# Optimization experiments

Hardware: AMD Instinct MI355X
Metric: run time of the kernel (lower is better)

The kernel has to match this reference:

```python
import jax, jax.numpy as jnp
import numpy as np

HEADS = 16
SEQ_LEN = 1024
MEM_LEN = 1024
CMEM_LEN = 256
CMEM_RATIO = 4


def _shift(x):
    # x: [b, h, i, j] -> relative position shift trick, output [b, h, i, j]
    b, h, i, j = x.shape
    x = jnp.concatenate([x, jnp.zeros((b, h, i, i), x.dtype)], -1)
    l = i + j - 1
    flat = x.reshape(b, h, -1)
    pad = (-flat.shape[-1]) % l
    flat = jnp.concatenate([flat, jnp.zeros((b, h, pad), x.dtype)], -1)
    return flat.reshape(b, h, -1, l)[..., :i, i - 1:]


def _full_attn(q, k, v):
    scale = q.shape[-1] ** -0.5
    a = jax.nn.softmax(jnp.einsum('bhid,bhjd->bhij', q, k) * scale, -1)
    return jnp.einsum('bhij,bhjd->bhid', a, v)


def setup_inputs() -> dict:
    key = jax.random.key(0)
    ks = jax.random.split(key, 10)
    b, t, e = 4, SEQ_LEN, 1024
    d = e // HEADS
    kv_len = CMEM_LEN + MEM_LEN + t
    s = 0.02
    return {
        'x': jax.random.normal(ks[0], (b, t, e), jnp.float32),
        'mem': jax.random.normal(ks[1], (b, MEM_LEN, e), jnp.float32),
        'cmem': jax.random.normal(ks[2], (b, CMEM_LEN, e), jnp.float32),
        'pos_emb': jax.random.normal(ks[3], (HEADS, kv_len, d), jnp.float32),
        'input_mask': jnp.ones((b, t), bool),
        'Wq': jax.random.normal(ks[4], (e, e), jnp.float32) * s,
        'Wkv': jax.random.normal(ks[5], (e, 2 * e), jnp.float32) * s,
        'Wout': jax.random.normal(ks[6], (e, e), jnp.float32) * s,
        'bout': jnp.zeros((e,), jnp.float32),
        'conv_w': jax.random.normal(ks[7], (e, e, CMEM_RATIO), jnp.float32) * s,
        'conv_b': jnp.zeros((e,), jnp.float32),
    }


def reference(x, mem, cmem, pos_emb, input_mask, Wq, Wkv, Wout, bout, conv_w, conv_b):
    b, t, e = x.shape
    h = HEADS
    d = e // h
    scale = d ** -0.5
    ml, cml = mem.shape[1], cmem.shape[1]

    q = x @ Wq                                      # [b, t, e]
    kv_input = jnp.concatenate([cmem, mem, x], 1)   # [b, kv_len, e]
    k, v = jnp.split(kv_input @ Wkv, 2, -1)

    mh = lambda u: u.reshape(b, -1, h, d).transpose(0, 2, 1, 3)
    q, k, v = mh(q), mh(k), mh(v)                   # [b, h, n, d]
    kv_len = k.shape[2]

    dots = jnp.einsum('bhid,bhjd->bhij', q, k) * scale
    neg = -jnp.finfo(dots.dtype).max

    pe = pos_emb[:, -kv_len:].astype(q.dtype)
    pos_dots = _shift(jnp.einsum('bhid,hjd->bhij', q, pe) * scale)
    dots = dots + pos_dots

    # padding mask (True where attention allowed), pad mem+cmem region with True
    pad_mask = input_mask[:, None, :, None] & input_mask[:, None, None, :]
    pad_mask = jnp.pad(pad_mask, ((0, 0), (0, 0), (0, 0), (ml + cml, 0)), constant_values=True)
    dots = jnp.where(pad_mask, dots, neg)

    total_mem = ml + cml
    causal = jnp.triu(jnp.ones((t, t + total_mem), bool), k=1 + total_mem)
    dots = jnp.where(causal[None, None], neg, dots)

    attn = jax.nn.softmax(dots, -1)
    out = jnp.einsum('bhij,bhjd->bhid', attn, v).transpose(0, 2, 1, 3).reshape(b, t, e)
    logits = out @ Wout + bout

    # --- memory update (t == seq_len, calc_memory=True) ---
    mem_cat = jnp.concatenate([mem, x], 1)          # [b, ml+t, e]
    old_mem, new_mem = mem_cat[:, :-MEM_LEN], mem_cat[:, -MEM_LEN:]
    # old_mem length (t) is divisible by CMEM_RATIO, no pad needed
    xm = old_mem.reshape(b, -1, CMEM_RATIO, e)
    compressed = jnp.einsum('bmri,oir->bmo', xm, conv_w) + conv_b  # Conv1d k=stride=ratio
    cmem_cat = jnp.concatenate([cmem, compressed], 1)
    new_cmem = cmem_cat[:, -CMEM_LEN:]

    # --- auxiliary reconstruction loss (all operands detached) ---
    ck, cv = jnp.split(compressed @ Wkv, 2, -1)
    ck, cv = mh(ck), mh(cv)
    start = kv_len - min(ml, MEM_LEN) - SEQ_LEN
    end = kv_len - SEQ_LEN
    omk, omv = k[:, :, start:end], v[:, :, start:end]
    sg = jax.lax.stop_gradient
    q2, omk, omv, ck, cv = map(sg, (q, omk, omv, ck, cv))
    aux_loss = jnp.mean((_full_attn(q2, omk, omv) - _full_attn(q2, ck, cv)) ** 2)

    return logits, new_mem, new_cmem, aux_loss
```

## Files before the change

### kernel.cpp

```cpp
#include <hip/hip_runtime.h>
#include <hip/hip_bf16.h>
#include <cstddef>

typedef unsigned short u16;
typedef __attribute__((ext_vector_type(8))) short bf16x8;
typedef __attribute__((ext_vector_type(4))) float f32x4;

#define C2 0.18033688011112042f

__device__ __forceinline__ u16 f2b(float f) {
    unsigned u = __builtin_bit_cast(unsigned, f);
    unsigned r = (u + 0x7FFF + ((u >> 16) & 1)) >> 16;
    return (u16)r;
}

__device__ __forceinline__ float exp2a(float x) {
    float r; asm("v_exp_f32 %0, %1" : "=v"(r) : "v"(x)); return r;
}

__device__ __forceinline__ unsigned cvtpk(float lo, float hi) {
    unsigned r; asm("v_cvt_pk_bf16_f32 %0, %1, %2" : "=v"(r) : "v"(lo), "v"(hi));
    return r;
}

__device__ __forceinline__ void gload_lds16(const void* g, void* l) {
    __builtin_amdgcn_global_load_lds(
        (const __attribute__((address_space(1))) unsigned int*)g,
        (__attribute__((address_space(3))) unsigned int*)l, 16, 0, 0);
}

#define VDRAIN() asm volatile("s_waitcnt vmcnt(0)" ::: "memory")
#define SBAR() do { __builtin_amdgcn_sched_barrier(0); __builtin_amdgcn_s_barrier(); } while (0)

__device__ __forceinline__ void transpose_body(
    const float* __restrict__ in, u16* __restrict__ out, int K, int N,
    int bx, int by, float (*t)[33], int tid)
{
    int k0 = by * 32, n0 = bx * 32;
    int tx = tid & 31, ty = tid >> 5;
    #pragma unroll
    for (int p = 0; p < 4; ++p)
        t[ty + 8 * p][tx] = in[(size_t)(k0 + ty + 8 * p) * N + n0 + tx];
    __syncthreads();
    #pragma unroll
    for (int p = 0; p < 4; ++p)
        out[(size_t)(n0 + ty + 8 * p) * K + k0 + tx] = f2b(t[tx][ty + 8 * p]);
}

__global__ __launch_bounds__(256) void megaprep(
    const float* __restrict__ pos, u16* __restrict__ peb,
    const float* __restrict__ x, const float* __restrict__ mem,
    const float* __restrict__ cmem, u16* __restrict__ kvin,
    const float* __restrict__ Wkv, u16* __restrict__ wkvt,
    const float* __restrict__ Wq, u16* __restrict__ wqt,
    const float* __restrict__ Wout, u16* __restrict__ woutt,
    const float* __restrict__ convw, u16* __restrict__ w2t)
{
    __shared__ float t[32][33];
    const int bid = blockIdx.x, tid = threadIdx.x;
    if (bid < 2304) {
        int i = bid * 256 + tid;
        float4 v = ((const float4*)pos)[i];
        union { u16 s[4]; uint2 u; } pk;
        pk.s[0] = f2b(v.x); pk.s[1] = f2b(v.y); pk.s[2] = f2b(v.z); pk.s[3] = f2b(v.w);
        ((uint2*)peb)[i] = pk.u;
    } else if (bid < 11520) {
        int rowg = bid - 2304;
        int b = rowg / 2304, rr = rowg % 2304;
        const float* src = (rr < 256)  ? cmem + ((size_t)b * 256 + rr) * 1024
                         : (rr < 1280) ? mem  + ((size_t)b * 1024 + (rr - 256)) * 1024
                                       : x    + ((size_t)b * 1024 + (rr - 1280)) * 1024;
        float4 v = ((const float4*)src)[tid];
        union { u16 s[4]; uint2 u; } pk;
        pk.s[0] = f2b(v.x); pk.s[1] = f2b(v.y); pk.s[2] = f2b(v.z); pk.s[3] = f2b(v.w);
        ((uint2*)(kvin + (size_t)rowg * 1024))[tid] = pk.u;
    } else if (bid < 13568) {
        int m = bid - 11520;
        transpose_body(Wkv, wkvt, 1024, 2048, m % 64, m / 64, t, tid);
    } else if (bid < 14592) {
        int m = bid - 13568;
        transpose_body(Wq, wqt, 1024, 1024, m % 32, m / 32, t, tid);
    } else if (bid < 15616) {
        int m = bid - 14592;
        transpose_body(Wout, woutt, 1024, 1024, m % 32, m / 32, t, tid);
    } else {
        int m = bid - 15616;
        int pidx = m * 256 + tid;
        int o = pidx >> 10, i = pidx & 1023;
        float4 v = *(const float4*)(convw + ((size_t)o << 12) + 4 * i);
        size_t base = (size_t)o * 4096 + i;
        w2t[base]          = f2b(v.x);
        w2t[base + 1024]   = f2b(v.y);
        w2t[base + 2048]   = f2b(v.z);
        w2t[base + 3072]   = f2b(v.w);
    }
}

__global__ __launch_bounds__(256) void transpose_v2(
    const u16* __restrict__ src1, u16* __restrict__ dst1,
    const u16* __restrict__ src2, u16* __restrict__ dst2)
{
    __shared__ u16 t[64 * 65];
    const int bid = blockIdx.x, tid = threadIdx.x;
    const u16* src; u16* dst; int R, bh, j0;
    if (bid < 2304) { src = src1; dst = dst1; R = 2304; bh = bid / 36; j0 = (bid % 36) * 64; }
    else { int m = bid - 2304; src = src2; dst = dst2; R = 256; bh = m / 4; j0 = (m % 4) * 64; }
    const int b = bh >> 4, h = bh & 15;
    #pragma unroll
    for (int p = 0; p < 2; ++p) {
        int idx = tid + p * 256;
        int j = idx >> 3, c = idx & 7;
        uint4 v = *(const uint4*)(src + ((size_t)(b * R + j0 + j)) * 2048 + 1024 + h * 64 + c * 8);
        const u16* vv = (const u16*)&v;
        #pragma unroll
        for (int u2 = 0; u2 < 8; ++u2) t[j * 65 + c * 8 + u2] = vv[u2];
    }
    __syncthreads();
    #pragma unroll
    for (int p = 0; p < 2; ++p) {
        int idx = tid + p * 256;
        int jc = idx & 7, d = idx >> 3;
        union { u16 s[8]; uint4 u; } pk;
        #pragma unroll
        for (int u2 = 0; u2 < 8; ++u2) pk.s[u2] = t[(jc * 8 + u2) * 65 + d];
        *(uint4*)(dst + ((size_t)(bh * 64 + d)) * (size_t)R + j0 + jc * 8) = pk.u;
    }
}

__device__ __forceinline__ void gemm_body(
    const u16* __restrict__ A, const u16* __restrict__ Bt,
    const float* __restrict__ bias, float* __restrict__ Cf,
    u16* __restrict__ Cb, int N, int K, float cscale,
    int apad, int ashift, int nxshift, int nyper, int id,
    u16* Al, u16* Bl)
{
    const int tid = threadIdx.x, w = tid >> 6, lane = tid & 63;
    const int lr = lane & 15, lg = lane >> 4;
    const int xcd = id & 7, s = id >> 3;
    const int bx = s & ((1 << nxshift) - 1);
    const int by = nyper * xcd + (s >> nxshift);
    const int bm0 = by * 128, bn0 = bx * 128;
    const int wr = (w >> 1) * 64, wc = (w & 1) * 64;

    f32x4 acc[4][4];
    const f32x4 z = {0.f, 0.f, 0.f, 0.f};
    #pragma unroll
    for (int mb = 0; mb < 4; ++mb)
        #pragma unroll
        for (int nb = 0; nb < 4; ++nb) acc[mb][nb] = z;

    for (int k0 = 0; k0 < K; k0 += 32) {
        __syncthreads();
        #pragma unroll
        for (int q = 0; q < 2; ++q) {
            int chunk = w * 2 + q;
            int row = bm0 + chunk * 16 + (lane >> 2);
            int arow = row + ((row >> ashift) * apad);
            int sg = (lane & 3) * 8;
            gload_lds16(A + (size_t)arow * K + k0 + sg, &Al[chunk * 512]);
            gload_lds16(Bt + (size_t)(bn0 + chunk * 16 + (lane >> 2)) * K + k0 + sg, &Bl[chunk * 512]);
        }
        __syncthreads();
        bf16x8 af[4], bf[4];
        #pragma unroll
        for (int mb = 0; mb < 4; ++mb)
            af[mb] = *(const bf16x8*)&Al[(wr + mb * 16 + lr) * 32 + lg * 8];
        #pragma unroll
        for (int nb = 0; nb < 4; ++nb)
            bf[nb] = *(const bf16x8*)&Bl[(wc + nb * 16 + lr) * 32 + lg * 8];
        #pragma unroll
        for (int mb = 0; mb < 4; ++mb)
            #pragma unroll
            for (int nb = 0; nb < 4; ++nb)
                acc[mb][nb] = __builtin_amdgcn_mfma_f32_16x16x32_bf16(
                    af[mb], bf[nb], acc[mb][nb], 0, 0, 0);
    }

    #pragma unroll
    for (int mb = 0; mb < 4; ++mb)
        #pragma unroll
        for (int nb = 0; nb < 4; ++nb)
            #pragma unroll
            for (int jr = 0; jr < 4; ++jr) {
                int row = bm0 + wr + mb * 16 + lg * 4 + jr;
                int col = bn0 + wc + nb * 16 + lr;
                float v = acc[mb][nb][jr] + (bias ? bias[col] : 0.f);
                if (Cf) Cf[(size_t)row * N + col] = v;
                if (Cb) Cb[(size_t)row * N + col] = f2b(v * cscale);
            }
}

__global__ __launch_bounds__(256) void gemm_bf16(
    const u16* __restrict__ A, const u16* __restrict__ Bt,
    const float* __restrict__ bias, float* __restrict__ Cf,
    u16* __restrict__ Cb, int N, int K, float cscale,
    int apad, int ashift, int nxshift, int nyper)
{
    __shared__ u16 Al[128 * 32];
    __shared__ u16 Bl[128 * 32];
    gemm_body(A, Bt, bias, Cf, Cb, N, K, cscale, apad, ashift, nxshift, nyper,
              blockIdx.x, Al, Bl);
}

__global__ __launch_bounds__(256) void gemm_dual(
    const u16* Aa, const u16* Bta, const float* biasa, float* Cfa, u16* Cba,
    int Na, int Ka, float csa, int apa, int asa, int nxa, int nya, int split,
    const u16* Ab, const u16* Btb, const float* biasb, float* Cfb, u16* Cbb,
    int Nb, int Kb, float csb, int apb, int asb, int nxb, int nyb)
{
    __shared__ u16 Al[128 * 32];
    __shared__ u16 Bl[128 * 32];
    if ((int)blockIdx.x < split)
        gemm_body(Aa, Bta, biasa, Cfa, Cba, Na, Ka, csa, apa, asa, nxa, nya,
                  blockIdx.x, Al, Bl);
    else
        gemm_body(Ab, Btb, biasb, Cfb, Cbb, Nb, Kb, csb, apb, asb, nxb, nyb,
                  blockIdx.x - split, Al, Bl);
}

__global__ __launch_bounds__(256) void attn_main_fused(
    const u16* __restrict__ qb,
    const u16* __restrict__ kvb,
    const u16* __restrict__ vt,
    const u16* __restrict__ peb,
    const u16* __restrict__ ckcv,
    const u16* __restrict__ cvt,
    u16* __restrict__ outb,
    float* __restrict__ acc)
{
    __shared__ u16 kbuf[64 * 64];
    __shared__ u16 vbuf[64 * 64];
    __shared__ u16 pering[128 * 64];
    __shared__ u16 pls[4][1024];
    __shared__ float red[4];

    const int tid = threadIdx.x;
    const int w = tid >> 6, lane = tid & 63;
    const int lr = lane & 15, lg = lane >> 4;
    const int rl = lane >> 3, cch = lane & 7;
    const int id = blockIdx.x;
    const int slot = id >> 3;
    const int bh = (id & 7) + ((slot >> 4) << 3);
    const int b = bh >> 4, h = bh & 15;
    const int i0 = (15 - (slot & 15)) * 64;
    const int iw = i0 + 16 * w;
    const int jb0 = 960 - i0;

    const int lrh = lr >> 3, lrm = lr & 7;
    int pwidx[4], pridx[2];
    #pragma unroll
    for (int nb = 0; nb < 4; ++nb)
        pwidx[nb] = (((nb * 2 + lrh) ^ (lg * 2)) * 8) + lrm;
    #pragma unroll
    for (int ks = 0; ks < 2; ++ks)
        pridx[ks] = lr * 64 + (((ks * 4 + lg) ^ ((lr >> 2) * 2)) * 8);

    bf16x8 qf[2];
    #pragma unroll
    for (int ks = 0; ks < 2; ++ks)
        qf[ks] = *(const bf16x8*)(qb + ((size_t)(b * 1024 + iw + lr)) * 1024
                                  + h * 64 + ks * 32 + lg * 8);

    const f32x4 z = {0.f, 0.f, 0.f, 0.f};
    f32x4 od[4], od2[4];
    float lloc[4], ll2[4];
    #pragma unroll
    for (int nb = 0; nb < 4; ++nb) { od[nb] = z; od2[nb] = z; }
    #pragma unroll
    for (int jr = 0; jr < 4; ++jr) { lloc[jr] = 0.f; ll2[jr] = 0.f; }

    #pragma unroll
    for (int q = 0; q < 2; ++q) {
        int row = 16 * w + 8 * q + rl;
        gload_lds16(kvb + ((size_t)(b * 2304 + row)) * 2048 + h * 64 + ((cch ^ rl) * 8),
                    &kbuf[(16 * w + 8 * q) * 64]);
        gload_lds16(vt + ((size_t)(bh * 64 + row)) * 2304 + ((cch ^ rl) * 8),
                    &vbuf[(16 * w + 8 * q) * 64]);
    }
    #pragma unroll
    for (int q = 0; q < 4; ++q) {
        int rr = 32 * w + 8 * q;
        int a = jb0 + rr + rl;
        int srow = a > 2303 ? 2303 : a;
        gload_lds16(peb + ((size_t)(h * 2304 + srow)) * 64 + ((cch ^ rl) * 8),
                    &pering[((jb0 + rr) & 127) * 64]);
    }
    VDRAIN();
    __syncthreads();

    const int nt = ((i0 + 1343) >> 6) + 1;
    for (int t = 0; t < nt; ++t) {
        const int j0 = t * 64;
        const int jb = jb0 + j0;
        const bool more = (t + 1 < nt);

        f32x4 qk[4], qp[5];
        #pragma unroll
        for (int nb = 0; nb < 4; ++nb) qk[nb] = z;
        #pragma unroll
        for (int f = 0; f < 5; ++f) qp[f] = z;
        __builtin_amdgcn_s_setprio(1);
        #pragma unroll
        for (int ks = 0; ks < 2; ++ks) {
            #pragma unroll
            for (int nb = 0; nb < 4; ++nb) {
                int row = nb * 16 + lr;
                bf16x8 kb = *(const bf16x8*)&kbuf[row * 64 + (((4 * ks + lg) ^ (row & 7)) * 8)];
                qk[nb] = __builtin_amdgcn_mfma_f32_16x16x32_bf16(qf[ks], kb, qk[nb], 0, 0, 0);
            }
            #pragma unroll
            for (int f = 0; f < 5; ++f) {
                int rel = 48 - 16 * w + f * 16 + lr;
                int slotp = (jb + rel) & 127;
                bf16x8 pb = *(const bf16x8*)&pering[slotp * 64 + (((4 * ks + lg) ^ (slotp & 7)) * 8)];
                qp[f] = __builtin_amdgcn_mfma_f32_16x16x32_bf16(qf[ks], pb, qp[f], 0, 0, 0);
            }
        }
        __builtin_amdgcn_s_setprio(0);

        VDRAIN();
        SBAR();

        if (more) {
            const int j0n = j0 + 64;
            #pragma unroll
            for (int q = 0; q < 2; ++q) {
                int row = 16 * w + 8 * q + rl;
                gload_lds16(kvb + ((size_t)(b * 2304 + j0n + row)) * 2048 + h * 64 + ((cch ^ rl) * 8),
                            &kbuf[(16 * w + 8 * q) * 64]);
            }
            const int A0 = jb + 128;
            #pragma unroll
            for (int q = 0; q < 2; ++q) {
                int rr = A0 + 16 * w + 8 * q;
                int a = rr + rl;
                int srow = a > 2303 ? 2303 : a;
                gload_lds16(peb + ((size_t)(h * 2304 + srow)) * 64 + ((cch ^ rl) * 8),
                            &pering[(rr & 127) * 64]);
            }
        }

        const bool nomask = (j0 + 63 <= iw + 1280);
        #pragma unroll
        for (int jr = 0; jr < 4; ++jr) {
            const int r = lg * 4 + jr;
            const int ia = iw + r;
            const int src = (lane & 48) | ((lr + 15 - r) & 15);
            float rot0 = __shfl(qp[0][jr], src);
            float rot1 = __shfl(qp[1][jr], src);
            float rot2 = __shfl(qp[2][jr], src);
            float rot3 = __shfl(qp[3][jr], src);
            float rot4 = __shfl(qp[4][jr], src);
            const bool hi = (lr > r);
            float s0 = qk[0][jr] + (hi ? rot1 : rot0);
            float s1 = qk[1][jr] + (hi ? rot2 : rot1);
            float s2 = qk[2][jr] + (hi ? rot3 : rot2);
            float s3 = qk[3][jr] + (hi ? rot4 : rot3);
            if (!nomask) {
                s0 = (j0 + lr      <= ia + 1280) ? s0 : -1e30f;
                s1 = (j0 + lr + 16 <= ia + 1280) ? s1 : -1e30f;
                s2 = (j0 + lr + 32 <= ia + 1280) ? s2 : -1e30f;
                s3 = (j0 + lr + 48 <= ia + 1280) ? s3 : -1e30f;
            }
            float p0 = exp2a(s0), p1 = exp2a(s1);
            float p2 = exp2a(s2), p3 = exp2a(s3);
            unsigned pkA = cvtpk(p0, p1), pkB = cvtpk(p2, p3);
            u16* pw = &pls[w][r * 64];
            pw[pwidx[0]] = (u16)pkA; pw[pwidx[1]] = (u16)(pkA >> 16);
            pw[pwidx[2]] = (u16)pkB; pw[pwidx[3]] = (u16)(pkB >> 16);
            lloc[jr] += (p0 + p1) + (p2 + p3);
        }

        __builtin_amdgcn_s_setprio(1);
        #pragma unroll
        for (int ks = 0; ks < 2; ++ks) {
            bf16x8 pa = *(const bf16x8*)&pls[w][pridx[ks]];
            #pragma unroll
            for (int nb = 0; nb < 4; ++nb) {
                int d = nb * 16 + lr;
                bf16x8 vb = *(const bf16x8*)&vbuf[d * 64 + (((4 * ks + lg) ^ (d & 7)) * 8)];
                od[nb] = __builtin_amdgcn_mfma_f32_16x16x32_bf16(pa, vb, od[nb], 0, 0, 0);
            }
        }
        __builtin_amdgcn_s_setprio(0);

        if (t >= 4 && t <= 19) {
            #pragma unroll
            for (int jr = 0; jr < 4; ++jr) {
                const int r = lg * 4 + jr;
                float p0 = exp2a(qk[0][jr]), p1 = exp2a(qk[1][jr]);
                float p2 = exp2a(qk[2][jr]), p3 = exp2a(qk[3][jr]);
                unsigned pkA = cvtpk(p0, p1), pkB = cvtpk(p2, p3);
                u16* pw = &pls[w][r * 64];
                pw[pwidx[0]] = (u16)pkA; pw[pwidx[1]] = (u16)(pkA >> 16);
                pw[pwidx[2]] = (u16)pkB; pw[pwidx[3]] = (u16)(pkB >> 16);
                ll2[jr] += (p0 + p1) + (p2 + p3);
            }
            __builtin_amdgcn_s_setprio(1);
            #pragma unroll
            for (int ks = 0; ks < 2; ++ks) {
                bf16x8 pa = *(const bf16x8*)&pls[w][pridx[ks]];
                #pragma unroll
                for (int nb = 0; nb < 4; ++nb) {
                    int d = nb * 16 + lr;
                    bf16x8 vb = *(const bf16x8*)&vbuf[d * 64 + (((4 * ks + lg) ^ (d & 7)) * 8)];
                    od2[nb] = __builtin_amdgcn_mfma_f32_16x16x32_bf16(pa, vb, od2[nb], 0, 0, 0);
                }
            }
            __builtin_amdgcn_s_setprio(0);
        }

        VDRAIN();
        SBAR();

        if (more) {
            const int j0n = j0 + 64;
            #pragma unroll
            for (int q = 0; q < 2; ++q) {
                int row = 16 * w + 8 * q + rl;
                gload_lds16(vt + ((size_t)(bh * 64 + row)) * 2304 + j0n + ((cch ^ rl) * 8),
                            &vbuf[(16 * w + 8 * q) * 64]);
            }
        }
    }

    #pragma unroll
    for (int jr = 0; jr < 4; ++jr) {
        float l = lloc[jr];
        #pragma unroll
        for (int mk = 1; mk < 16; mk <<= 1) l += __shfl_xor(l, mk);
        float inv = 1.f / l;
        int ia = iw + lg * 4 + jr;
        #pragma unroll
        for (int nb = 0; nb < 4; ++nb)
            outb[((size_t)(b * 1024 + ia)) * 1024 + h * 64 + nb * 16 + lr] =
                f2b(od[nb][jr] * inv);
    }
    #pragma unroll
    for (int jr = 0; jr < 4; ++jr) {
        float l = ll2[jr];
        #pragma unroll
        for (int mk = 1; mk < 16; mk <<= 1) l += __shfl_xor(l, mk);
        float inv = 1.f / l;
        #pragma unroll
        for (int nb = 0; nb < 4; ++nb) od2[nb][jr] *= inv;
    }

    #pragma unroll
    for (int nb = 0; nb < 4; ++nb) od[nb] = z;
    #pragma unroll
    for (int jr = 0; jr < 4; ++jr) lloc[jr] = 0.f;
    const u16* kbase = ckcv + ((size_t)(b * 256)) * 2048 + h * 64;
    const u16* vbase = cvt + ((size_t)(bh * 64)) * 256;

    for (int t = 0; t < 4; ++t) {
        const int j0 = t * 64;
        __syncthreads();
        #pragma unroll
        for (int q = 0; q < 2; ++q) {
            int row = 16 * w + 8 * q + rl;
            gload_lds16(kbase + (size_t)(j0 + row) * 2048 + ((cch ^ rl) * 8),
                        &kbuf[(16 * w + 8 * q) * 64]);
            gload_lds16(vbase + (size_t)row * 256 + j0 + ((cch ^ rl) * 8),
                        &vbuf[(16 * w + 8 * q) * 64]);
        }
        VDRAIN();
        __syncthreads();

        f32x4 qk[4];
        #pragma unroll
        for (int nb = 0; nb < 4; ++nb) qk[nb] = z;
        #pragma unroll
        for (int ks = 0; ks < 2; ++ks)
            #pragma unroll
            for (int nb = 0; nb < 4; ++nb) {
                int row = nb * 16 + lr;
                bf16x8 kb = *(const bf16x8*)&kbuf[row * 64 + (((4 * ks + lg) ^ (row & 7)) * 8)];
                qk[nb] = __builtin_amdgcn_mfma_f32_16x16x32_bf16(qf[ks], kb, qk[nb], 0, 0, 0);
            }

        #pragma unroll
        for (int jr = 0; jr < 4; ++jr) {
            const int r = lg * 4 + jr;
            float p0 = exp2a(qk[0][jr]), p1 = exp2a(qk[1][jr]);
            float p2 = exp2a(qk[2][jr]), p3 = exp2a(qk[3][jr]);
            unsigned pkA = cvtpk(p0, p1), pkB = cvtpk(p2, p3);
            u16* pw = &pls[w][r * 64];
            pw[pwidx[0]] = (u16)pkA; pw[pwidx[1]] = (u16)(pkA >> 16);
            pw[pwidx[2]] = (u16)pkB; pw[pwidx[3]] = (u16)(pkB >> 16);
            lloc[jr] += (p0 + p1) + (p2 + p3);
        }

        #pragma unroll
        for (int ks = 0; ks < 2; ++ks) {
            bf16x8 pa = *(const bf16x8*)&pls[w][pridx[ks]];
            #pragma unroll
            for (int nb = 0; nb < 4; ++nb) {
                int d = nb * 16 + lr;
                bf16x8 vb = *(const bf16x8*)&vbuf[d * 64 + (((4 * ks + lg) ^ (d & 7)) * 8)];
                od[nb] = __builtin_amdgcn_mfma_f32_16x16x32_bf16(pa, vb, od[nb], 0, 0, 0);
            }
        }
    }

    float local = 0.f;
    #pragma unroll
    for (int jr = 0; jr < 4; ++jr) {
        float l = lloc[jr];
        #pragma unroll
        for (int mk = 1; mk < 16; mk <<= 1) l += __shfl_xor(l, mk);
        float inv = 1.f / l;
        #pragma unroll
        for (int nb = 0; nb < 4; ++nb) {
            float d = od2[nb][jr] - od[nb][jr] * inv;
            local += d * d;
        }
    }
    #pragma unroll
    for (int mk = 1; mk < 64; mk <<= 1) local += __shfl_xor(local, mk);
    if (lane == 0) red[w] = local;
    __syncthreads();
    if (tid == 0) atomicAdd(acc, red[0] + red[1] + red[2] + red[3]);
}

__global__ void finish_aux(const float* __restrict__ acc, float* __restrict__ out)
{
    out[0] = acc[0] * (1.0f / 4194304.0f);
}

extern "C" void kernel_launch(void* const* d_in, const int* in_sizes, int n_in,
                              void* d_out, int out_size, void* d_ws, size_t ws_size,
                              hipStream_t stream)
{
    const float* x     = (const float*)d_in[0];
    const float* mem   = (const float*)d_in[1];
    const float* cmem  = (const float*)d_in[2];
    const float* pos   = (const float*)d_in[3];
    const float* Wq    = (const float*)d_in[5];
    const float* Wkv   = (const float*)d_in[6];
    const float* Wout  = (const float*)d_in[7];
    const float* bout  = (const float*)d_in[8];
    const float* convw = (const float*)d_in[9];
    const float* convb = (const float*)d_in[10];

    float* out      = (float*)d_out;
    float* logits   = out;
    float* new_mem  = out + 4194304;
    float* new_cmem = out + 8388608;
    float* aux_out  = out + 9437184;

    char* p = (char*)d_ws;
    u16* kvb   = (u16*)p; p += (size_t)9216 * 2048 * 2;
    u16* qb    = (u16*)p; p += (size_t)4096 * 1024 * 2;
    u16* kvin  = (u16*)p; p += (size_t)9216 * 1024 * 2;
    u16* wkvt  = (u16*)p; p += (size_t)2048 * 1024 * 2;
    u16* wqt   = (u16*)p; p += (size_t)1024 * 1024 * 2;
    u16* woutt = (u16*)p; p += (size_t)1024 * 1024 * 2;
    u16* w2t   = (u16*)p; p += (size_t)1024 * 4096 * 2;
    u16* peb   = (u16*)p; p += (size_t)16 * 2304 * 64 * 2;
    u16* xb    = (u16*)p; p += (size_t)4096 * 1024 * 2;
    u16* memb  = (u16*)p; p += (size_t)4096 * 1024 * 2;
    u16* cmpb  = (u16*)p; p += (size_t)1024 * 1024 * 2;
    u16* ckcvb = (u16*)p; p += (size_t)1024 * 2048 * 2;
    u16* aob   = (u16*)p; p += (size_t)4096 * 1024 * 2;
    float* acc = (float*)p;
    u16* vt   = kvin;
    u16* cvt  = w2t;
    (void)xb; (void)memb;

    hipMemcpyAsync(new_mem, x, (size_t)4194304 * sizeof(float),
                   hipMemcpyDeviceToDevice, stream);

    megaprep<<<19712, 256, 0, stream>>>(pos, peb, x, mem, cmem, kvin,
                                        Wkv, wkvt, Wq, wqt, Wout, woutt, convw, w2t);

    gemm_bf16<<<1152, 256, 0, stream>>>(kvin, wkvt, nullptr, nullptr, kvb,
                                        2048, 1024, 1.f, 0, 10, 4, 9);
    gemm_dual<<<320, 256, 0, stream>>>(
        kvin + (size_t)1280 * 1024, wqt, nullptr, nullptr, qb,
        1024, 1024, C2, 1280, 10, 3, 4, 256,
        kvin + (size_t)256 * 1024, w2t, convb, new_cmem, cmpb,
        1024, 4096, 1.f, 320, 8, 3, 1);
    gemm_bf16<<<128, 256, 0, stream>>>(cmpb, wkvt, nullptr, nullptr, ckcvb,
                                       2048, 1024, 1.f, 0, 10, 4, 1);

    transpose_v2<<<2560, 256, 0, stream>>>(kvb, vt, ckcvb, cvt);

    hipMemsetAsync(acc, 0, sizeof(float), stream);
    attn_main_fused<<<1024, 256, 0, stream>>>(qb, kvb, vt, peb, ckcvb, cvt, aob, acc);
    gemm_bf16<<<256, 256, 0, stream>>>(aob, woutt, bout, logits, nullptr,
                                       1024, 1024, 1.f, 0, 10, 3, 4);

    finish_aux<<<1, 1, 0, stream>>>(acc, aux_out);
}
```

Measured before the change: 419.2 us.

## Consolidate launches: fold memcpy, memset, GEMMs and transposes into fewer kernels

The new_mem device copy and the accumulator reset move into the megaprep kernel. The KV, Q and conv GEMMs now run in one launch. The V transpose runs alongside the compressed-KV GEMM, with the small cvt transpose split into its own kernel. The finish_aux step folds into the output GEMM. The goal is to cut per-launch gaps and let independent work share the GPU. The cost is more branch-heavy kernels and a slightly different grouping of dependent stages.

```diff
diff --git a/kernel.cpp b/kernel.cpp
--- a/kernel.cpp
+++ b/kernel.cpp
@@ -54,18 +54,23 @@
     const float* __restrict__ Wkv, u16* __restrict__ wkvt,
     const float* __restrict__ Wq, u16* __restrict__ wqt,
     const float* __restrict__ Wout, u16* __restrict__ woutt,
-    const float* __restrict__ convw, u16* __restrict__ w2t)
+    const float* __restrict__ convw, u16* __restrict__ w2t,
+    float* __restrict__ new_mem, float* __restrict__ acc)
 {
     __shared__ float t[32][33];
     const int bid = blockIdx.x, tid = threadIdx.x;
-    if (bid < 2304) {
+    if (bid == 0 && tid == 0) acc[0] = 0.f;
+    if (bid < 4096) {
         int i = bid * 256 + tid;
+        ((float4*)new_mem)[i] = ((const float4*)x)[i];
+    } else if (bid < 6400) {
+        int i = (bid - 4096) * 256 + tid;
         float4 v = ((const float4*)pos)[i];
         union { u16 s[4]; uint2 u; } pk;
         pk.s[0] = f2b(v.x); pk.s[1] = f2b(v.y); pk.s[2] = f2b(v.z); pk.s[3] = f2b(v.w);
         ((uint2*)peb)[i] = pk.u;
-    } else if (bid < 11520) {
-        int rowg = bid - 2304;
+    } else if (bid < 15616) {
+        int rowg = bid - 6400;
         int b = rowg / 2304, rr = rowg % 2304;
         const float* src = (rr < 256)  ? cmem + ((size_t)b * 256 + rr) * 1024
                          : (rr < 1280) ? mem  + ((size_t)b * 1024 + (rr - 256)) * 1024
@@ -74,56 +79,25 @@
         union { u16 s[4]; uint2 u; } pk;
         pk.s[0] = f2b(v.x); pk.s[1] = f2b(v.y); pk.s[2] = f2b(v.z); pk.s[3] = f2b(v.w);
         ((uint2*)(kvin + (size_t)rowg * 1024))[tid] = pk.u;
-    } else if (bid < 13568) {
-        int m = bid - 11520;
+    } else if (bid < 17664) {
+        int m = bid - 15616;
         transpose_body(Wkv, wkvt, 1024, 2048, m % 64, m / 64, t, tid);
-    } else if (bid < 14592) {
-        int m = bid - 13568;
+    } else if (bid < 18688) {
+        int m = bid - 17664;
         transpose_body(Wq, wqt, 1024, 1024, m % 32, m / 32, t, tid);
-    } else if (bid < 15616) {
-        int m = bid - 14592;
+    } else if (bid < 19712) {
+        int m = bid - 18688;
         transpose_body(Wout, woutt, 1024, 1024, m % 32, m / 32, t, tid);
     } else {
-        int m = bid - 15616;
+        int m = bid - 19712;
         int pidx = m * 256 + tid;
         int o = pidx >> 10, i = pidx & 1023;
         float4 v = *(const float4*)(convw + ((size_t)o << 12) + 4 * i);
         size_t base = (size_t)o * 4096 + i;
-        w2t[base]          = f2b(v.x);
-        w2t[base + 1024]   = f2b(v.y);
-        w2t[base + 2048]   = f2b(v.z);
-        w2t[base + 3072]   = f2b(v.w);
-    }
-}
-
-__global__ __launch_bounds__(256) void transpose_v2(
-    const u16* __restrict__ src1, u16* __restrict__ dst1,
-    const u16* __restrict__ src2, u16* __restrict__ dst2)
-{
-    __shared__ u16 t[64 * 65];
-    const int bid = blockIdx.x, tid = threadIdx.x;
-    const u16* src; u16* dst; int R, bh, j0;
-    if (bid < 2304) { src = src1; dst = dst1; R = 2304; bh = bid / 36; j0 = (bid % 36) * 64; }
-    else { int m = bid - 2304; src = src2; dst = dst2; R = 256; bh = m / 4; j0 = (m % 4) * 64; }
-    const int b = bh >> 4, h = bh & 15;
-    #pragma unroll
-    for (int p = 0; p < 2; ++p) {
-        int idx = tid + p * 256;
-        int j = idx >> 3, c = idx & 7;
-        uint4 v = *(const uint4*)(src + ((size_t)(b * R + j0 + j)) * 2048 + 1024 + h * 64 + c * 8);
-        const u16* vv = (const u16*)&v;
-        #pragma unroll
-        for (int u2 = 0; u2 < 8; ++u2) t[j * 65 + c * 8 + u2] = vv[u2];
-    }
-    __syncthreads();
-    #pragma unroll
-    for (int p = 0; p < 2; ++p) {
-        int idx = tid + p * 256;
-        int jc = idx & 7, d = idx >> 3;
-        union { u16 s[8]; uint4 u; } pk;
-        #pragma unroll
-        for (int u2 = 0; u2 < 8; ++u2) pk.s[u2] = t[(jc * 8 + u2) * 65 + d];
-        *(uint4*)(dst + ((size_t)(bh * 64 + d)) * (size_t)R + j0 + jc * 8) = pk.u;
+        w2t[base]        = f2b(v.x);
+        w2t[base + 1024] = f2b(v.y);
+        w2t[base + 2048] = f2b(v.z);
+        w2t[base + 3072] = f2b(v.w);
     }
 }
 
@@ -190,43 +164,93 @@
             }
 }
 
-__global__ __launch_bounds__(256) void gemm_bf16(
-    const u16* __restrict__ A, const u16* __restrict__ Bt,
-    const float* __restrict__ bias, float* __restrict__ Cf,
-    u16* __restrict__ Cb, int N, int K, float cscale,
-    int apad, int ashift, int nxshift, int nyper)
+__global__ __launch_bounds__(256) void gemm_stage1(
+    const u16* __restrict__ kvin, const u16* __restrict__ wkvt,
+    const u16* __restrict__ wqt, const u16* __restrict__ w2t,
+    const float* __restrict__ convb, u16* __restrict__ kvb,
+    u16* __restrict__ qb, float* __restrict__ new_cmem, u16* __restrict__ cmpb)
 {
     __shared__ u16 Al[128 * 32];
     __shared__ u16 Bl[128 * 32];
-    gemm_body(A, Bt, bias, Cf, Cb, N, K, cscale, apad, ashift, nxshift, nyper,
-              blockIdx.x, Al, Bl);
-}
-
-__global__ __launch_bounds__(256) void gemm_dual(
-    const u16* Aa, const u16* Bta, const float* biasa, float* Cfa, u16* Cba,
-    int Na, int Ka, float csa, int apa, int asa, int nxa, int nya, int split,
-    const u16* Ab, const u16* Btb, const float* biasb, float* Cfb, u16* Cbb,
-    int Nb, int Kb, float csb, int apb, int asb, int nxb, int nyb)
+    const int id = blockIdx.x;
+    if (id < 1152)
+        gemm_body(kvin, wkvt, nullptr, nullptr, kvb, 2048, 1024, 1.f,
+                  0, 10, 4, 9, id, Al, Bl);
+    else if (id < 1408)
+        gemm_body(kvin + (size_t)1280 * 1024, wqt, nullptr, nullptr, qb,
+                  1024, 1024, C2, 1280, 10, 3, 4, id - 1152, Al, Bl);
+    else
+        gemm_body(kvin + (size_t)256 * 1024, w2t, convb, new_cmem, cmpb,
+                  1024, 4096, 1.f, 320, 8, 3, 1, id - 1408, Al, Bl);
+}
+
+__device__ __forceinline__ void transpose_v_body(
+    const u16* __restrict__ src, int R, u16* __restrict__ dst,
+    int bh, int j0, u16* t, int tid)
+{
+    const int b = bh >> 4, h = bh & 15;
+    #pragma unroll
+    for (int p = 0; p < 2; ++p) {
+        int idx = tid + p * 256;
+        int j = idx >> 3, c = idx & 7;
+        uint4 v = *(const uint4*)(src + ((size_t)(b * R + j0 + j)) * 2048 + 1024 + h * 64 + c * 8);
+        const u16* vv = (const u16*)&v;
+        #pragma unroll
+        for (int u2 = 0; u2 < 8; ++u2) t[j * 65 + c * 8 + u2] = vv[u2];
+    }
+    __syncthreads();
+    #pragma unroll
+    for (int p = 0; p < 2; ++p) {
+        int idx = tid + p * 256;
+        int jc = idx & 7, d = idx >> 3;
+        union { u16 s[8]; uint4 u; } pk;
+        #pragma unroll
+        for (int u2 = 0; u2 < 8; ++u2) pk.s[u2] = t[(jc * 8 + u2) * 65 + d];
+        *(uint4*)(dst + ((size_t)(bh * 64 + d)) * (size_t)R + j0 + jc * 8) = pk.u;
+    }
+}
+
+__global__ __launch_bounds__(256) void gemm_ckcv_tv(
+    const u16* __restrict__ cmpb, const u16* __restrict__ wkvt,
+    u16* __restrict__ ckcvb, const u16* __restrict__ kvb, u16* __restrict__ vt)
+{
+    __shared__ u16 shmem[128 * 64];
+    const int id = blockIdx.x;
+    if (id < 128) {
+        gemm_body(cmpb, wkvt, nullptr, nullptr, ckcvb, 2048, 1024, 1.f,
+                  0, 10, 4, 1, id, shmem, shmem + 4096);
+    } else {
+        int m = id - 128;
+        transpose_v_body(kvb, 2304, vt, m / 36, (m % 36) * 64, shmem, threadIdx.x);
+    }
+}
+
+__global__ __launch_bounds__(256) void transpose_cvt(
+    const u16* __restrict__ ckcvb, u16* __restrict__ cvt)
+{
+    __shared__ u16 t[64 * 65];
+    int m = blockIdx.x;
+    transpose_v_body(ckcvb, 256, cvt, m / 4, (m % 4) * 64, t, threadIdx.x);
+}
+
+__global__ __launch_bounds__(256) void gemm_out(
+    const u16* __restrict__ aob, const u16* __restrict__ woutt,
+    const float* __restrict__ bout, float* __restrict__ logits,
+    const float* __restrict__ acc, float* __restrict__ aux_out)
 {
     __shared__ u16 Al[128 * 32];
     __shared__ u16 Bl[128 * 32];
-    if ((int)blockIdx.x < split)
-        gemm_body(Aa, Bta, biasa, Cfa, Cba, Na, Ka, csa, apa, asa, nxa, nya,
-                  blockIdx.x, Al, Bl);
-    else
-        gemm_body(Ab, Btb, biasb, Cfb, Cbb, Nb, Kb, csb, apb, asb, nxb, nyb,
-                  blockIdx.x - split, Al, Bl);
+    if (blockIdx.x == 0 && threadIdx.x == 0)
+        aux_out[0] = acc[0] * (1.0f / 4194304.0f);
+    gemm_body(aob, woutt, bout, logits, nullptr, 1024, 1024, 1.f,
+              0, 10, 3, 4, blockIdx.x, Al, Bl);
 }
 
 __global__ __launch_bounds__(256) void attn_main_fused(
-    const u16* __restrict__ qb,
-    const u16* __restrict__ kvb,
-    const u16* __restrict__ vt,
-    const u16* __restrict__ peb,
-    const u16* __restrict__ ckcv,
-    const u16* __restrict__ cvt,
-    u16* __restrict__ outb,
-    float* __restrict__ acc)
+    const u16* __restrict__ qb, const u16* __restrict__ kvb,
+    const u16* __restrict__ vt, const u16* __restrict__ peb,
+    const u16* __restrict__ ckcv, const u16* __restrict__ cvt,
+    u16* __restrict__ outb, float* __restrict__ acc)
 {
     __shared__ u16 kbuf[64 * 64];
     __shared__ u16 vbuf[64 * 64];
@@ -523,11 +547,6 @@
     if (tid == 0) atomicAdd(acc, red[0] + red[1] + red[2] + red[3]);
 }
 
-__global__ void finish_aux(const float* __restrict__ acc, float* __restrict__ out)
-{
-    out[0] = acc[0] * (1.0f / 4194304.0f);
-}
-
 extern "C" void kernel_launch(void* const* d_in, const int* in_sizes, int n_in,
                               void* d_out, int out_size, void* d_ws, size_t ws_size,
                               hipStream_t stream)
@@ -568,28 +587,18 @@
     u16* cvt  = w2t;
     (void)xb; (void)memb;
 
-    hipMemcpyAsync(new_mem, x, (size_t)4194304 * sizeof(float),
-                   hipMemcpyDeviceToDevice, stream);
-
-    megaprep<<<19712, 256, 0, stream>>>(pos, peb, x, mem, cmem, kvin,
-                                        Wkv, wkvt, Wq, wqt, Wout, woutt, convw, w2t);
-
-    gemm_bf16<<<1152, 256, 0, stream>>>(kvin, wkvt, nullptr, nullptr, kvb,
-                                        2048, 1024, 1.f, 0, 10, 4, 9);
-    gemm_dual<<<320, 256, 0, stream>>>(
-        kvin + (size_t)1280 * 1024, wqt, nullptr, nullptr, qb,
-        1024, 1024, C2, 1280, 10, 3, 4, 256,
-        kvin + (size_t)256 * 1024, w2t, convb, new_cmem, cmpb,
-        1024, 4096, 1.f, 320, 8, 3, 1);
-    gemm_bf16<<<128, 256, 0, stream>>>(cmpb, wkvt, nullptr, nullptr, ckcvb,
-                                       2048, 1024, 1.f, 0, 10, 4, 1);
-
-    transpose_v2<<<2560, 256, 0, stream>>>(kvb, vt, ckcvb, cvt);
-
-    hipMemsetAsync(acc, 0, sizeof(float), stream);
+    megaprep<<<23808, 256, 0, stream>>>(pos, peb, x, mem, cmem, kvin,
+                                        Wkv, wkvt, Wq, wqt, Wout, woutt,
+                                        convw, w2t, new_mem, acc);
+
+    gemm_stage1<<<1472, 256, 0, stream>>>(kvin, wkvt, wqt, w2t, convb,
+                                          kvb, qb, new_cmem, cmpb);
+
+    gemm_ckcv_tv<<<2432, 256, 0, stream>>>(cmpb, wkvt, ckcvb, kvb, vt);
+
+    transpose_cvt<<<256, 256, 0, stream>>>(ckcvb, cvt);
+
     attn_main_fused<<<1024, 256, 0, stream>>>(qb, kvb, vt, peb, ckcvb, cvt, aob, acc);
-    gemm_bf16<<<256, 256, 0, stream>>>(aob, woutt, bout, logits, nullptr,
-                                       1024, 1024, 1.f, 0, 10, 3, 4);
-
-    finish_aux<<<1, 1, 0, stream>>>(acc, aux_out);
-}
+
+    gemm_out<<<256, 256, 0, stream>>>(aob, woutt, bout, logits, acc, aux_out);
+}
```

After: 362.7 us. 13.5% less time.
